# Kernel optimization log

Hardware: AMD Instinct MI355X
Metric: run time of the kernel (lower is better)

Reference implementation:

```python
import jax, jax.numpy as jnp
import numpy as np

NUM_HEADS = 8
HEAD_DIM = 64
INPUT_DIM = 512
OUT_DIM = 512
INNER_DIM = NUM_HEADS * HEAD_DIM


def setup_inputs() -> dict:
    key = jax.random.key(0)
    ks = jax.random.split(key, 5)
    B, T = 4, 2048
    x = jax.random.normal(ks[0], (B, T, INPUT_DIM), dtype=jnp.float32)
    Wk = jax.random.normal(ks[1], (INNER_DIM, INPUT_DIM), dtype=jnp.float32)
    Wq = jax.random.normal(ks[2], (INNER_DIM, INPUT_DIM), dtype=jnp.float32)
    Wv = jax.random.normal(ks[3], (INNER_DIM, INPUT_DIM), dtype=jnp.float32)
    Wp = jax.random.normal(ks[4], (OUT_DIM, INNER_DIM), dtype=jnp.float32)
    return {"x": x, "Wk": Wk, "Wq": Wq, "Wv": Wv, "Wp": Wp, "causal_mask": 0}


def reference(x, Wk, Wq, Wv, Wp, causal_mask):
    B, T, C = x.shape
    c_scale = C ** (-0.5)

    def proj(W):
        # (B,T,C) @ (C,inner) -> (B,T,H,D) -> (B,H,T,D), scaled by C^-0.5
        return (jnp.einsum('btc,ic->bti', x, W)
                .reshape(B, T, NUM_HEADS, HEAD_DIM)
                .transpose(0, 2, 1, 3) * c_scale)

    q, k, v = proj(Wq), proj(Wk), proj(Wv)
    # scores: (B,H,T,T), scaled by head_dim^-0.5
    weight = jnp.einsum('bhqd,bhkd->bhqk', q, k) * (HEAD_DIM ** (-0.5))
    if causal_mask:
        mask = jnp.triu(jnp.ones((T, T), dtype=bool), k=1)
        weight = jnp.where(mask, -jnp.inf, weight)
    weight = jax.nn.softmax(weight, axis=-1)
    out = jnp.einsum('bhqk,bhkd->bhqd', weight, v)  # (B,H,T,D)
    out = out.transpose(0, 2, 1, 3).reshape(B, T, INNER_DIM)
    # final projection scaled by inner_dim^-0.5 (projection.size(-1))
    out = jnp.einsum('bti,oi->bto', out, Wp) * (INNER_DIM ** (-0.5))
    return out
```

## Files before the change

### kernel.cpp

```cpp
#include <hip/hip_runtime.h>
#include <stdint.h>

#define T_SEQ 2048
#define NB 4
#define NH 8
#define DH 64
#define CD 512

typedef __attribute__((ext_vector_type(8))) short bf16x8;
typedef __attribute__((ext_vector_type(4))) uint16_t u16x4;
typedef __attribute__((ext_vector_type(4))) float f32x4;
typedef __attribute__((ext_vector_type(16))) float f32x16;
typedef __attribute__((ext_vector_type(4))) int i32x4;

#if __has_builtin(__builtin_amdgcn_exp2f)
#define EXP2(x) __builtin_amdgcn_exp2f(x)
#else
#define EXP2(x) exp2f(x)
#endif

__device__ __forceinline__ uint16_t f2bf(float f) {
  uint32_t u = __float_as_uint(f);
  u += 0x7FFFu + ((u >> 16) & 1u);
  return (uint16_t)(u >> 16);
}

__device__ __forceinline__ uint32_t cvtpk_bf16(float lo, float hi) {
  uint32_t r;
  asm("v_cvt_pk_bf16_f32 %0, %1, %2" : "=v"(r) : "v"(lo), "v"(hi));
  return r;
}

__device__ __forceinline__ void gload_lds16(const void* g, void* l) {
  __builtin_amdgcn_global_load_lds((const __attribute__((address_space(1))) void*)g,
                                   (__attribute__((address_space(3))) void*)l, 16, 0, 0);
}

__global__ __launch_bounds__(256) void cvt_all(const float* __restrict__ x,
    const float* __restrict__ wq, const float* __restrict__ wk,
    const float* __restrict__ wv, const float* __restrict__ wp,
    uint16_t* __restrict__ ws) {
  int i = blockIdx.x * 256 + threadIdx.x;
  int e = i * 4;
  const float* src;
  uint16_t* dst;
  if (e < 4194304) {
    src = x + e; dst = ws + e;
  } else {
    int r = e - 4194304;
    int w = r >> 18;
    int o = r & 262143;
    const float* W = (w == 0) ? wq : (w == 1) ? wk : (w == 2) ? wv : wp;
    src = W + o;
    dst = ws + 4194304 + (w << 18) + o;
  }
  float4 v = *(const float4*)src;
  u16x4 o4 = { f2bf(v.x), f2bf(v.y), f2bf(v.z), f2bf(v.w) };
  *(u16x4*)dst = o4;
}

__device__ __forceinline__ void gemm_bt_tile(const uint16_t* __restrict__ A,
                                             const uint16_t* __restrict__ Bt,
                                             int m0, int n0,
                                             uint16_t* As, uint16_t* Bs,
                                             f32x4 acc[4][4]) {
  const int tid = threadIdx.x;
  const int lane = tid & 63;
  const int wave = tid >> 6;
  const int wr = (wave >> 1) * 64, wc = (wave & 1) * 64;
  const int l15 = lane & 15, l4 = lane >> 4;

#pragma unroll
  for (int m = 0; m < 4; ++m)
#pragma unroll
    for (int n = 0; n < 4; ++n)
      acc[m][n] = (f32x4){0.f, 0.f, 0.f, 0.f};

  for (int kt = 0; kt < 8; ++kt) {
#pragma unroll
    for (int is = 0; is < 4; ++is) {
      int p = is * 4096 + tid * 16;
      int g = p ^ (((p >> 7) & 7) << 4);
      int row = g >> 7, colb = g & 127;
      gload_lds16((const char*)A + (size_t)(m0 + row) * 1024 + kt * 128 + colb,
                  (char*)As + p);
      gload_lds16((const char*)Bt + (size_t)(n0 + row) * 1024 + kt * 128 + colb,
                  (char*)Bs + p);
    }
    __syncthreads();
#pragma unroll
    for (int ks = 0; ks < 2; ++ks) {
      bf16x8 af[4], bfr[4];
#pragma unroll
      for (int m = 0; m < 4; ++m) {
        int row = wr + m * 16 + l15;
        int byt = (row * 128 + ks * 64 + l4 * 16) ^ ((row & 7) << 4);
        af[m] = *(const bf16x8*)((const char*)As + byt);
      }
#pragma unroll
      for (int n = 0; n < 4; ++n) {
        int row = wc + n * 16 + l15;
        int byt = (row * 128 + ks * 64 + l4 * 16) ^ ((row & 7) << 4);
        bfr[n] = *(const bf16x8*)((const char*)Bs + byt);
      }
#pragma unroll
      for (int m = 0; m < 4; ++m)
#pragma unroll
        for (int n = 0; n < 4; ++n)
          acc[m][n] = __builtin_amdgcn_mfma_f32_16x16x32_bf16(af[m], bfr[n], acc[m][n], 0, 0, 0);
    }
    __syncthreads();
  }
}

__global__ __launch_bounds__(256) void proj_kernel(const uint16_t* __restrict__ xb,
    const uint16_t* __restrict__ wbase, uint16_t* __restrict__ qkv,
    float qscale, float kvscale) {
  __shared__ __align__(16) uint16_t As[128 * 64];
  __shared__ __align__(16) uint16_t Bs[128 * 64];
  int z = blockIdx.z;
  const uint16_t* W = wbase + (size_t)z * 262144;
  uint16_t* outb = qkv + (size_t)z * 4194304;
  float scale = (z == 0) ? qscale : kvscale;
  f32x4 acc[4][4];
  int lane = threadIdx.x & 63, wave = threadIdx.x >> 6;
  int wr = (wave >> 1) * 64, wc = (wave & 1) * 64;
  int l15 = lane & 15, l4 = lane >> 4;

  if (z < 2) {
    int m0 = blockIdx.x * 128, n0 = blockIdx.y * 128;
    gemm_bt_tile(xb, W, m0, n0, As, Bs, acc);
#pragma unroll
    for (int m = 0; m < 4; ++m)
#pragma unroll
      for (int n = 0; n < 4; ++n)
#pragma unroll
        for (int j = 0; j < 4; ++j) {
          int row = m0 + wr + m * 16 + l4 * 4 + j;
          int col = n0 + wc + n * 16 + l15;
          int b = row >> 11, t = row & 2047;
          int h = col >> 6, d = col & 63;
          outb[((size_t)(b * NH + h) * T_SEQ + t) * DH + d] = f2bf(acc[m][n][j] * scale);
        }
  } else {
    int m0 = blockIdx.y * 128, n0 = blockIdx.x * 128;
    gemm_bt_tile(W, xb, m0, n0, As, Bs, acc);
#pragma unroll
    for (int m = 0; m < 4; ++m)
#pragma unroll
      for (int n = 0; n < 4; ++n)
#pragma unroll
        for (int j = 0; j < 4; ++j) {
          int row = m0 + wr + m * 16 + l4 * 4 + j;
          int col = n0 + wc + n * 16 + l15;
          int h = row >> 6, d = row & 63;
          int b = col >> 11, t = col & 2047;
          outb[((size_t)(b * NH + h) * DH + d) * T_SEQ + t] = f2bf(acc[m][n][j] * scale);
        }
  }
}

__global__ __launch_bounds__(256) void attn3(const uint16_t* __restrict__ Q,
    const uint16_t* __restrict__ K, const uint16_t* __restrict__ VT,
    uint16_t* __restrict__ AO) {
  __shared__ __align__(16) uint16_t Ka[4][4096];
  __shared__ __align__(16) uint16_t Va[4][4096];

  int bid = blockIdx.x;
  int swz = (bid & 7) * 64 + (bid >> 3);
  int qt = swz & 15, bh = swz >> 4;
  int b = bh >> 3, h = bh & 7;
  int tid = threadIdx.x, lane = tid & 63, wave = tid >> 6;
  int l31 = lane & 31, hi = lane >> 5;

  const uint16_t* Kb  = K  + (size_t)bh * T_SEQ * DH;
  const uint16_t* VTb = VT + (size_t)bh * DH * T_SEQ;
  const uint16_t* Qrow = Q + ((size_t)bh * T_SEQ + qt * 128 + wave * 32 + l31) * DH;

  auto stage = [&](int t) {
    int bufi = t & 3;
    const char* ksrc = (const char*)Kb + (size_t)t * 8192;
#pragma unroll
    for (int c = 0; c < 2; ++c) {
      int p = c * 4096 + tid * 16;
      int g = p ^ (((p >> 7) & 7) << 4);
      gload_lds16(ksrc + g, (char*)(&Ka[bufi][0]) + p);
      int row = g >> 7, off = g & 127;
      gload_lds16((const char*)VTb + (size_t)row * 4096 + (size_t)t * 128 + off,
                  (char*)(&Va[bufi][0]) + p);
    }
  };

  bf16x8 qf[4];
#pragma unroll
  for (int m = 0; m < 4; ++m)
    qf[m] = *(const bf16x8*)((const char*)Qrow + m * 32 + hi * 16);

  f32x16 Oacc[2];
#pragma unroll
  for (int dB = 0; dB < 2; ++dB) Oacc[dB] = (f32x16)(0.f);
  float lp0 = 0.f, lp1 = 0.f, lp2 = 0.f, lp3 = 0.f;

  stage(0);
  stage(1);

  for (int kt = 0; kt < 32; ++kt) {
    if (kt + 2 < 32) stage(kt + 2);

    if (kt < 30)       asm volatile("s_waitcnt vmcnt(8)\n\ts_barrier" ::: "memory");
    else if (kt == 30) asm volatile("s_waitcnt vmcnt(4)\n\ts_barrier" ::: "memory");
    else               asm volatile("s_waitcnt vmcnt(0)\n\ts_barrier" ::: "memory");

    const char* Kc = (const char*)(&Ka[kt & 3][0]);
    const char* Vc = (const char*)(&Va[kt & 3][0]);

    f32x16 s0 = (f32x16)(0.f), s1 = (f32x16)(0.f);
    __builtin_amdgcn_s_setprio(1);
#pragma unroll
    for (int m = 0; m < 4; ++m) {
      int row0 = l31;
      int byt0 = (row0 * 128 + m * 32 + hi * 16) ^ ((row0 & 7) << 4);
      bf16x8 kf0 = *(const bf16x8*)(Kc + byt0);
      s0 = __builtin_amdgcn_mfma_f32_32x32x16_bf16(kf0, qf[m], s0, 0, 0, 0);
      int row1 = 32 + l31;
      int byt1 = (row1 * 128 + m * 32 + hi * 16) ^ ((row1 & 7) << 4);
      bf16x8 kf1 = *(const bf16x8*)(Kc + byt1);
      s1 = __builtin_amdgcn_mfma_f32_32x32x16_bf16(kf1, qf[m], s1, 0, 0, 0);
    }
    __builtin_amdgcn_s_setprio(0);

    uint32_t pa_[2][4], pb_[2][4];
    {
      float e0[16], e1[16];
#pragma unroll
      for (int r = 0; r < 16; ++r) e0[r] = EXP2(s0[r]);
#pragma unroll
      for (int r = 0; r < 16; ++r) e1[r] = EXP2(s1[r]);
#pragma unroll
      for (int r = 0; r < 16; ++r) {
        if ((r & 3) == 0)      { lp0 += e0[r]; lp0 += e1[r]; }
        else if ((r & 3) == 1) { lp1 += e0[r]; lp1 += e1[r]; }
        else if ((r & 3) == 2) { lp2 += e0[r]; lp2 += e1[r]; }
        else                   { lp3 += e0[r]; lp3 += e1[r]; }
      }
#pragma unroll
      for (int g = 0; g < 4; ++g) {
        pa_[0][g] = cvtpk_bf16(e0[4 * g], e0[4 * g + 1]);
        pb_[0][g] = cvtpk_bf16(e0[4 * g + 2], e0[4 * g + 3]);
        pa_[1][g] = cvtpk_bf16(e1[4 * g], e1[4 * g + 1]);
        pb_[1][g] = cvtpk_bf16(e1[4 * g + 2], e1[4 * g + 3]);
      }
    }

#pragma unroll
    for (int km = 0; km < 4; ++km) {
      const int Tt = km >> 1;
      const int g0 = (km & 1) * 2;
      uint32_t w0 = pa_[Tt][g0], w2 = pa_[Tt][g0 + 1];
      uint32_t w1 = pb_[Tt][g0], w3 = pb_[Tt][g0 + 1];
      asm volatile("v_permlane32_swap_b32 %0, %1" : "+v"(w0), "+v"(w2));
      asm volatile("v_permlane32_swap_b32 %0, %1" : "+v"(w1), "+v"(w3));
      i32x4 pw = { (int)w0, (int)w1, (int)w2, (int)w3 };
      bf16x8 paf = __builtin_bit_cast(bf16x8, pw);
      __builtin_amdgcn_s_setprio(1);
#pragma unroll
      for (int dB = 0; dB < 2; ++dB) {
        int row = dB * 32 + l31;
        int byt = (row * 128 + km * 32 + hi * 16) ^ ((row & 7) << 4);
        bf16x8 vf = *(const bf16x8*)(Vc + byt);
        Oacc[dB] = __builtin_amdgcn_mfma_f32_32x32x16_bf16(paf, vf, Oacc[dB], 0, 0, 0);
      }
      __builtin_amdgcn_s_setprio(0);
    }
  }

  float lpart = (lp0 + lp1) + (lp2 + lp3);
  float lsum = lpart + __shfl_xor(lpart, 32, 64);
  float inv = 1.f / lsum;
  int qb0 = qt * 128 + wave * 32;
#pragma unroll
  for (int r = 0; r < 16; ++r) {
    int qoff = (r & 3) + 8 * (r >> 2) + 4 * hi;
    float invr = __shfl(inv, qoff, 64);
    int t = qb0 + qoff;
    size_t base = ((size_t)(b * T_SEQ + t)) * 512 + h * 64;
    AO[base + l31]      = f2bf(Oacc[0][r] * invr);
    AO[base + 32 + l31] = f2bf(Oacc[1][r] * invr);
  }
}

__global__ __launch_bounds__(256) void final_kernel(const uint16_t* __restrict__ ab,
    const uint16_t* __restrict__ wpb, float* __restrict__ out, float scale) {
  __shared__ __align__(16) uint16_t As[128 * 64];
  __shared__ __align__(16) uint16_t Bs[128 * 64];
  int m0 = blockIdx.x * 128, n0 = blockIdx.y * 128;
  f32x4 acc[4][4];
  gemm_bt_tile(ab, wpb, m0, n0, As, Bs, acc);
  int lane = threadIdx.x & 63, wave = threadIdx.x >> 6;
  int wr = (wave >> 1) * 64, wc = (wave & 1) * 64;
  int l15 = lane & 15, l4 = lane >> 4;
#pragma unroll
  for (int m = 0; m < 4; ++m)
#pragma unroll
    for (int n = 0; n < 4; ++n)
#pragma unroll
      for (int j = 0; j < 4; ++j) {
        int row = m0 + wr + m * 16 + l4 * 4 + j;
        int col = n0 + wc + n * 16 + l15;
        out[(size_t)row * 512 + col] = acc[m][n][j] * scale;
      }
}

extern "C" void kernel_launch(void* const* d_in, const int* in_sizes, int n_in,
                              void* d_out, int out_size, void* d_ws, size_t ws_size,
                              hipStream_t stream) {
  const float* x  = (const float*)d_in[0];
  const float* Wk = (const float*)d_in[1];
  const float* Wq = (const float*)d_in[2];
  const float* Wv = (const float*)d_in[3];
  const float* Wp = (const float*)d_in[4];
  uint16_t* ws = (uint16_t*)d_ws;

  uint16_t* xb  = ws;
  uint16_t* wqb = ws + 4194304;
  uint16_t* qkv = ws + 4194304 + 4 * 262144;
  uint16_t* qb  = qkv;
  uint16_t* kb  = qkv + 4194304;
  uint16_t* vtb = qkv + 2 * 4194304;
  uint16_t* ao  = xb;
  uint16_t* wpb = wqb + 3 * 262144;

  const float c_scale = 0.04419417382415922f;
  const float qscale = c_scale * 0.125f * 1.4426950408889634f;
  const float fscale = c_scale;

  cvt_all<<<dim3(5120), dim3(256), 0, stream>>>(x, Wq, Wk, Wv, Wp, ws);
  proj_kernel<<<dim3(64, 4, 3), dim3(256), 0, stream>>>(xb, wqb, qkv, qscale, c_scale);
  attn3<<<dim3(512), dim3(256), 0, stream>>>(qb, kb, vtb, ao);
  final_kernel<<<dim3(64, 4), dim3(256), 0, stream>>>(ao, wpb, (float*)d_out, fscale);
}
```

Before: 98.94 us.

## Split attention KV range across two wave groups and merge partial outputs

The attention block grows to 512 threads. Two groups of four waves each process half of the key/value sequence for the same 128 queries, each with a double-buffered LDS stage. Partial output accumulators and row sums are combined through shared memory at the end, which works without max rescaling because the kernel uses no running max. This doubles the waves per block to improve latency hiding and shortens each wave's serial loop, at the cost of an extra barrier per iteration, shallower prefetch and a reduction through LDS.

```diff
diff --git a/kernel.cpp b/kernel.cpp
--- a/kernel.cpp
+++ b/kernel.cpp
@@ -160,11 +160,10 @@
   }
 }
 
-__global__ __launch_bounds__(256) void attn3(const uint16_t* __restrict__ Q,
+__global__ __launch_bounds__(512, 4) void attn5(const uint16_t* __restrict__ Q,
     const uint16_t* __restrict__ K, const uint16_t* __restrict__ VT,
     uint16_t* __restrict__ AO) {
-  __shared__ __align__(16) uint16_t Ka[4][4096];
-  __shared__ __align__(16) uint16_t Va[4][4096];
+  __shared__ __align__(16) char smem[65536];
 
   int bid = blockIdx.x;
   int swz = (bid & 7) * 64 + (bid >> 3);
@@ -172,22 +171,26 @@
   int b = bh >> 3, h = bh & 7;
   int tid = threadIdx.x, lane = tid & 63, wave = tid >> 6;
   int l31 = lane & 31, hi = lane >> 5;
-
-  const uint16_t* Kb  = K  + (size_t)bh * T_SEQ * DH;
-  const uint16_t* VTb = VT + (size_t)bh * DH * T_SEQ;
-  const uint16_t* Qrow = Q + ((size_t)bh * T_SEQ + qt * 128 + wave * 32 + l31) * DH;
+  int p = tid >> 8;
+  int tin = tid & 255;
+  int w4 = wave & 3;
+
+  const char* Kb  = (const char*)(K  + (size_t)bh * T_SEQ * DH) + (size_t)p * 131072;
+  const char* VTb = (const char*)(VT + (size_t)bh * DH * T_SEQ);
+  const uint16_t* Qrow = Q + ((size_t)bh * T_SEQ + qt * 128 + w4 * 32 + l31) * DH;
+  char* pbase = smem + p * 32768;
 
   auto stage = [&](int t) {
-    int bufi = t & 3;
-    const char* ksrc = (const char*)Kb + (size_t)t * 8192;
+    char* kd = pbase + (t & 1) * 8192;
+    char* vd = pbase + 16384 + (t & 1) * 8192;
+    const char* ksrc = Kb + (size_t)t * 8192;
 #pragma unroll
     for (int c = 0; c < 2; ++c) {
-      int p = c * 4096 + tid * 16;
-      int g = p ^ (((p >> 7) & 7) << 4);
-      gload_lds16(ksrc + g, (char*)(&Ka[bufi][0]) + p);
+      int pp = c * 4096 + tin * 16;
+      int g = pp ^ (((pp >> 7) & 7) << 4);
+      gload_lds16(ksrc + g, kd + pp);
       int row = g >> 7, off = g & 127;
-      gload_lds16((const char*)VTb + (size_t)row * 4096 + (size_t)t * 128 + off,
-                  (char*)(&Va[bufi][0]) + p);
+      gload_lds16(VTb + (size_t)row * 4096 + p * 2048 + (size_t)t * 128 + off, vd + pp);
     }
   };
 
@@ -202,17 +205,14 @@
   float lp0 = 0.f, lp1 = 0.f, lp2 = 0.f, lp3 = 0.f;
 
   stage(0);
-  stage(1);
-
-  for (int kt = 0; kt < 32; ++kt) {
-    if (kt + 2 < 32) stage(kt + 2);
-
-    if (kt < 30)       asm volatile("s_waitcnt vmcnt(8)\n\ts_barrier" ::: "memory");
-    else if (kt == 30) asm volatile("s_waitcnt vmcnt(4)\n\ts_barrier" ::: "memory");
-    else               asm volatile("s_waitcnt vmcnt(0)\n\ts_barrier" ::: "memory");
-
-    const char* Kc = (const char*)(&Ka[kt & 3][0]);
-    const char* Vc = (const char*)(&Va[kt & 3][0]);
+
+  for (int kt = 0; kt < 16; ++kt) {
+    if (kt + 1 < 16) stage(kt + 1);
+    if (kt + 1 < 16) asm volatile("s_waitcnt vmcnt(4)\n\ts_barrier" ::: "memory");
+    else             asm volatile("s_waitcnt vmcnt(0)\n\ts_barrier" ::: "memory");
+
+    const char* Kc = pbase + (kt & 1) * 8192;
+    const char* Vc = pbase + 16384 + (kt & 1) * 8192;
 
     f32x16 s0 = (f32x16)(0.f), s1 = (f32x16)(0.f);
     __builtin_amdgcn_s_setprio(1);
@@ -272,20 +272,41 @@
       }
       __builtin_amdgcn_s_setprio(0);
     }
+
+    asm volatile("s_waitcnt lgkmcnt(0)\n\ts_barrier" ::: "memory");
   }
 
   float lpart = (lp0 + lp1) + (lp2 + lp3);
   float lsum = lpart + __shfl_xor(lpart, 32, 64);
-  float inv = 1.f / lsum;
-  int qb0 = qt * 128 + wave * 32;
-#pragma unroll
-  for (int r = 0; r < 16; ++r) {
-    int qoff = (r & 3) + 8 * (r >> 2) + 4 * hi;
-    float invr = __shfl(inv, qoff, 64);
-    int t = qb0 + qoff;
-    size_t base = ((size_t)(b * T_SEQ + t)) * 512 + h * 64;
-    AO[base + l31]      = f2bf(Oacc[0][r] * invr);
-    AO[base + 32 + l31] = f2bf(Oacc[1][r] * invr);
+  float* cm = (float*)smem;
+  float* slot = cm + (size_t)w4 * 2112 + lane * 33;
+  if (p == 1) {
+#pragma unroll
+    for (int dB = 0; dB < 2; ++dB)
+#pragma unroll
+      for (int r = 0; r < 16; ++r)
+        slot[dB * 16 + r] = Oacc[dB][r];
+    slot[32] = lsum;
+  }
+  __syncthreads();
+  if (p == 0) {
+    float inv = 1.f / (lsum + slot[32]);
+    f32x16 o0, o1;
+#pragma unroll
+    for (int r = 0; r < 16; ++r) {
+      o0[r] = Oacc[0][r] + slot[r];
+      o1[r] = Oacc[1][r] + slot[16 + r];
+    }
+    int qb0 = qt * 128 + w4 * 32;
+#pragma unroll
+    for (int r = 0; r < 16; ++r) {
+      int qoff = (r & 3) + 8 * (r >> 2) + 4 * hi;
+      float invr = __shfl(inv, qoff, 64);
+      int t = qb0 + qoff;
+      size_t base = ((size_t)(b * T_SEQ + t)) * 512 + h * 64;
+      AO[base + l31]      = f2bf(o0[r] * invr);
+      AO[base + 32 + l31] = f2bf(o1[r] * invr);
+    }
   }
 }
 
@@ -336,6 +357,6 @@
 
   cvt_all<<<dim3(5120), dim3(256), 0, stream>>>(x, Wq, Wk, Wv, Wp, ws);
   proj_kernel<<<dim3(64, 4, 3), dim3(256), 0, stream>>>(xb, wqb, qkv, qscale, c_scale);
-  attn3<<<dim3(512), dim3(256), 0, stream>>>(qb, kb, vtb, ao);
+  attn5<<<dim3(512), dim3(512), 0, stream>>>(qb, kb, vtb, ao);
   final_kernel<<<dim3(64, 4), dim3(256), 0, stream>>>(ao, wpb, (float*)d_out, fscale);
 }
```

After: 91.25 us. 7.8% less time.

## Split attention along the key dimension into four partitions and combine afterwards

Applied to the files above, without the earlier changes.

The attention kernel now splits the key/value sequence into four chunks, launching four times as many blocks. Each block writes unnormalized bf16 partial outputs and row sums, and a new combine kernel adds them and normalizes. The staging also drops from a 4-deep to a 2-deep buffer with a full wait each iteration. This targets poor occupancy on the 512-block grid, at the cost of an extra kernel launch, extra global traffic for the partials, and extra bf16 rounding of the partial sums. Summing chunks without rescaling relies on there being no running max in the softmax, as before.

```diff
diff --git a/kernel.cpp b/kernel.cpp
--- a/kernel.cpp
+++ b/kernel.cpp
@@ -8,6 +8,7 @@
 #define CD 512
 
 typedef __attribute__((ext_vector_type(8))) short bf16x8;
+typedef __attribute__((ext_vector_type(8))) uint16_t u16x8;
 typedef __attribute__((ext_vector_type(4))) uint16_t u16x4;
 typedef __attribute__((ext_vector_type(4))) float f32x4;
 typedef __attribute__((ext_vector_type(16))) float f32x16;
@@ -23,6 +24,10 @@
   uint32_t u = __float_as_uint(f);
   u += 0x7FFFu + ((u >> 16) & 1u);
   return (uint16_t)(u >> 16);
+}
+
+__device__ __forceinline__ float bf2f(uint16_t u) {
+  return __uint_as_float(((uint32_t)u) << 16);
 }
 
 __device__ __forceinline__ uint32_t cvtpk_bf16(float lo, float hi) {
@@ -160,34 +165,34 @@
   }
 }
 
-__global__ __launch_bounds__(256) void attn3(const uint16_t* __restrict__ Q,
+__global__ __launch_bounds__(256) void attn8(const uint16_t* __restrict__ Q,
     const uint16_t* __restrict__ K, const uint16_t* __restrict__ VT,
-    uint16_t* __restrict__ AO) {
-  __shared__ __align__(16) uint16_t Ka[4][4096];
-  __shared__ __align__(16) uint16_t Va[4][4096];
+    uint16_t* __restrict__ Op, float* __restrict__ Lp) {
+  __shared__ __align__(16) char kbuf[2][8192];
+  __shared__ __align__(16) char vbuf[2][8192];
 
   int bid = blockIdx.x;
-  int swz = (bid & 7) * 64 + (bid >> 3);
-  int qt = swz & 15, bh = swz >> 4;
-  int b = bh >> 3, h = bh & 7;
+  int swz = (bid & 7) * 256 + (bid >> 3);
+  int qt = swz & 15, qtr = (swz >> 4) & 3, bh = swz >> 6;
   int tid = threadIdx.x, lane = tid & 63, wave = tid >> 6;
   int l31 = lane & 31, hi = lane >> 5;
 
-  const uint16_t* Kb  = K  + (size_t)bh * T_SEQ * DH;
-  const uint16_t* VTb = VT + (size_t)bh * DH * T_SEQ;
+  const char* Kb  = (const char*)(K + (size_t)bh * T_SEQ * DH) + (size_t)qtr * 65536;
+  const char* VTb = (const char*)(VT + (size_t)bh * DH * T_SEQ);
   const uint16_t* Qrow = Q + ((size_t)bh * T_SEQ + qt * 128 + wave * 32 + l31) * DH;
 
   auto stage = [&](int t) {
-    int bufi = t & 3;
-    const char* ksrc = (const char*)Kb + (size_t)t * 8192;
+    char* kd = &kbuf[t & 1][0];
+    char* vd = &vbuf[t & 1][0];
+    const char* ksrc = Kb + (size_t)t * 8192;
 #pragma unroll
     for (int c = 0; c < 2; ++c) {
-      int p = c * 4096 + tid * 16;
-      int g = p ^ (((p >> 7) & 7) << 4);
-      gload_lds16(ksrc + g, (char*)(&Ka[bufi][0]) + p);
+      int pp = c * 4096 + tid * 16;
+      int g = pp ^ (((pp >> 7) & 7) << 4);
+      gload_lds16(ksrc + g, kd + pp);
       int row = g >> 7, off = g & 127;
-      gload_lds16((const char*)VTb + (size_t)row * 4096 + (size_t)t * 128 + off,
-                  (char*)(&Va[bufi][0]) + p);
+      gload_lds16(VTb + (size_t)row * 4096 + qtr * 1024 + (size_t)t * 128 + off,
+                  vd + pp);
     }
   };
 
@@ -197,29 +202,24 @@
     qf[m] = *(const bf16x8*)((const char*)Qrow + m * 32 + hi * 16);
 
   f32x16 Oacc[2];
-#pragma unroll
-  for (int dB = 0; dB < 2; ++dB) Oacc[dB] = (f32x16)(0.f);
+  Oacc[0] = (f32x16)(0.f);
+  Oacc[1] = (f32x16)(0.f);
   float lp0 = 0.f, lp1 = 0.f, lp2 = 0.f, lp3 = 0.f;
 
   stage(0);
-  stage(1);
-
-  for (int kt = 0; kt < 32; ++kt) {
-    if (kt + 2 < 32) stage(kt + 2);
-
-    if (kt < 30)       asm volatile("s_waitcnt vmcnt(8)\n\ts_barrier" ::: "memory");
-    else if (kt == 30) asm volatile("s_waitcnt vmcnt(4)\n\ts_barrier" ::: "memory");
-    else               asm volatile("s_waitcnt vmcnt(0)\n\ts_barrier" ::: "memory");
-
-    const char* Kc = (const char*)(&Ka[kt & 3][0]);
-    const char* Vc = (const char*)(&Va[kt & 3][0]);
+
+  for (int kt = 0; kt < 8; ++kt) {
+    asm volatile("s_waitcnt vmcnt(0) lgkmcnt(0)\n\ts_barrier" ::: "memory");
+    if (kt + 1 < 8) stage(kt + 1);
+
+    const char* Kc = &kbuf[kt & 1][0];
+    const char* Vc = &vbuf[kt & 1][0];
 
     f32x16 s0 = (f32x16)(0.f), s1 = (f32x16)(0.f);
     __builtin_amdgcn_s_setprio(1);
 #pragma unroll
     for (int m = 0; m < 4; ++m) {
-      int row0 = l31;
-      int byt0 = (row0 * 128 + m * 32 + hi * 16) ^ ((row0 & 7) << 4);
+      int byt0 = (l31 * 128 + m * 32 + hi * 16) ^ ((l31 & 7) << 4);
       bf16x8 kf0 = *(const bf16x8*)(Kc + byt0);
       s0 = __builtin_amdgcn_mfma_f32_32x32x16_bf16(kf0, qf[m], s0, 0, 0, 0);
       int row1 = 32 + l31;
@@ -258,8 +258,8 @@
       const int g0 = (km & 1) * 2;
       uint32_t w0 = pa_[Tt][g0], w2 = pa_[Tt][g0 + 1];
       uint32_t w1 = pb_[Tt][g0], w3 = pb_[Tt][g0 + 1];
-      asm volatile("v_permlane32_swap_b32 %0, %1" : "+v"(w0), "+v"(w2));
-      asm volatile("v_permlane32_swap_b32 %0, %1" : "+v"(w1), "+v"(w3));
+      asm("v_permlane32_swap_b32 %0, %1" : "+v"(w0), "+v"(w2));
+      asm("v_permlane32_swap_b32 %0, %1" : "+v"(w1), "+v"(w3));
       i32x4 pw = { (int)w0, (int)w1, (int)w2, (int)w3 };
       bf16x8 paf = __builtin_bit_cast(bf16x8, pw);
       __builtin_amdgcn_s_setprio(1);
@@ -276,17 +276,36 @@
 
   float lpart = (lp0 + lp1) + (lp2 + lp3);
   float lsum = lpart + __shfl_xor(lpart, 32, 64);
-  float inv = 1.f / lsum;
-  int qb0 = qt * 128 + wave * 32;
+  int rowbase = bh * 2048 + qt * 128 + wave * 32;
+  if (hi == 0) Lp[qtr * 65536 + rowbase + l31] = lsum;
+  uint16_t* Oq = Op + (size_t)qtr * 65536 * 64;
 #pragma unroll
   for (int r = 0; r < 16; ++r) {
     int qoff = (r & 3) + 8 * (r >> 2) + 4 * hi;
-    float invr = __shfl(inv, qoff, 64);
-    int t = qb0 + qoff;
-    size_t base = ((size_t)(b * T_SEQ + t)) * 512 + h * 64;
-    AO[base + l31]      = f2bf(Oacc[0][r] * invr);
-    AO[base + 32 + l31] = f2bf(Oacc[1][r] * invr);
-  }
+    size_t ro = (size_t)(rowbase + qoff);
+    Oq[ro * 64 + l31]      = f2bf(Oacc[0][r]);
+    Oq[ro * 64 + 32 + l31] = f2bf(Oacc[1][r]);
+  }
+}
+
+__global__ __launch_bounds__(256) void combine4(const uint16_t* __restrict__ Op,
+    const float* __restrict__ Lp, uint16_t* __restrict__ ao) {
+  int idx = blockIdx.x * 256 + threadIdx.x;
+  int row = idx >> 3, d0 = (idx & 7) * 8;
+  float inv = 1.f / (Lp[row] + Lp[65536 + row] + Lp[131072 + row] + Lp[196608 + row]);
+  float acc[8] = {0.f, 0.f, 0.f, 0.f, 0.f, 0.f, 0.f, 0.f};
+#pragma unroll
+  for (int q = 0; q < 4; ++q) {
+    u16x8 v = *(const u16x8*)(Op + ((size_t)q * 65536 + row) * 64 + d0);
+#pragma unroll
+    for (int j = 0; j < 8; ++j) acc[j] += bf2f(v[j]);
+  }
+  int bh = row >> 11, t = row & 2047;
+  int b = bh >> 3, h = bh & 7;
+  u16x8 o;
+#pragma unroll
+  for (int j = 0; j < 8; ++j) o[j] = f2bf(acc[j] * inv);
+  *(u16x8*)(ao + ((size_t)(b * 2048 + t) * 512 + h * 64 + d0)) = o;
 }
 
 __global__ __launch_bounds__(256) void final_kernel(const uint16_t* __restrict__ ab,
@@ -330,12 +349,16 @@
   uint16_t* ao  = xb;
   uint16_t* wpb = wqb + 3 * 262144;
 
+  uint16_t* opart = ws + 17825792;
+  float*    lpart = (float*)(ws + 34603008);
+
   const float c_scale = 0.04419417382415922f;
   const float qscale = c_scale * 0.125f * 1.4426950408889634f;
   const float fscale = c_scale;
 
   cvt_all<<<dim3(5120), dim3(256), 0, stream>>>(x, Wq, Wk, Wv, Wp, ws);
   proj_kernel<<<dim3(64, 4, 3), dim3(256), 0, stream>>>(xb, wqb, qkv, qscale, c_scale);
-  attn3<<<dim3(512), dim3(256), 0, stream>>>(qb, kb, vtb, ao);
+  attn8<<<dim3(2048), dim3(256), 0, stream>>>(qb, kb, vtb, opart, lpart);
+  combine4<<<dim3(2048), dim3(256), 0, stream>>>(opart, lpart, ao);
   final_kernel<<<dim3(64, 4), dim3(256), 0, stream>>>(ao, wpb, (float*)d_out, fscale);
 }
```

After: 108.6 us. 1.1x slower.
